# Optimization experiments

Measured on AMD Instinct MI355X. Metric: run time of the kernel, lower is better.

Reference implementation:

```python
import jax, jax.numpy as jnp
import numpy as np

N_FILTERS = 1024
KH, KW = 5, 5
LOC = 3                      # locality (pad + maxpool kernel/stride)
B, H, W = 1024, 64, 64
WIN = KH + 2 * LOC           # 11: sliced window side after padding


def setup_inputs() -> dict:
    key = jax.random.key(0)
    k1, k2, k3, k4 = jax.random.split(key, 4)
    X = jax.random.normal(k1, (B, 1, H, W), dtype=jnp.float32)
    weight = jax.random.normal(k2, (N_FILTERS, 1, KH, KW), dtype=jnp.float32)
    bias = jax.random.normal(k3, (N_FILTERS,), dtype=jnp.float32)
    # top-left corner (i, j) of each filter's window in the padded image;
    # must satisfy i + KH + 2*LOC <= H + 2*LOC  =>  i in [0, H-KH]
    positions = jax.random.randint(k4, (N_FILTERS, 2), 0, H - KH + 1, dtype=jnp.int32)
    return {"X": X, "weight": weight, "bias": bias, "positions": positions}


def reference(X, weight, bias, positions):
    # ZeroPad2d(locality)
    Xp = jnp.pad(X, ((0, 0), (0, 0), (LOC, LOC), (LOC, LOC)))

    def slice_one(pos):
        return jax.lax.dynamic_slice(Xp, (0, 0, pos[0], pos[1]), (B, 1, WIN, WIN))

    windows = jax.vmap(slice_one)(positions)
    lhs = jnp.transpose(windows[:, :, 0], (1, 0, 2, 3))

    # All n_filters tiny single-channel convs as ONE grouped conv.
    conv = jax.lax.conv_general_dilated(
        lhs, weight, window_strides=(1, 1), padding='VALID',
        dimension_numbers=('NCHW', 'OIHW', 'NCHW'),
        feature_group_count=N_FILTERS)                # [B,F,2L+1,2L+1] = [B,F,7,7]
    conv = conv + bias[None, :, None, None]

    # MaxPool2d((LOC,LOC)) with default stride=LOC, floor mode -> 2x2.
    pooled = jax.lax.reduce_window(
        conv, -jnp.inf, jax.lax.max,
        window_dimensions=(1, 1, LOC, LOC),
        window_strides=(1, 1, LOC, LOC),
        padding='VALID')                              # [B,F,2,2]

    # torch.cat(dim=1) over per-filter [B,1,2,2] tensors + reshape(B,-1)
    return pooled.reshape(B, -1)                      # [B, F*4]
```

## Files before the change

### kernel.cpp

```cpp
#include <hip/hip_runtime.h>

#define N_FILTERS 1024
#define B_TOTAL   1024
#define IMG       64
#define PAD_DIM   70

__global__ void zero_border_kernel(_Float16* __restrict__ Xt) {
    int bid = blockIdx.x;
    int r, c;
    if (bid < 420) {
        int r6 = bid / 70;
        c = bid - r6 * 70;
        r = (r6 < 3) ? r6 : r6 + 64;
    } else {
        int t = bid - 420;
        r = 3 + t / 6;
        int k = t - (t / 6) * 6;
        c = (k < 3) ? k : k + 64;
    }
    const size_t pp = (size_t)r * PAD_DIM + c;
    const int bg = threadIdx.x >> 5, l = threadIdx.x & 31;
    unsigned long long* q = (unsigned long long*)Xt
        + (size_t)bg * (4900ull * 32) + pp * 32 + l;
    *q = 0ull;
}

__global__ __launch_bounds__(256) void transpose_kernel(
    const float* __restrict__ X, _Float16* __restrict__ Xt)
{
    __shared__ float T[64 * 65];
    const int pt = blockIdx.x & 63;
    const int bt = blockIdx.x >> 6;
    const int tx = threadIdx.x & 63, ty = threadIdx.x >> 6;

    #pragma unroll
    for (int pass = 0; pass < 16; ++pass) {
        int bl = pass * 4 + ty;
        T[bl * 65 + tx] = X[(size_t)(bt * 64 + bl) * 4096 + pt * 64 + tx];
    }
    __syncthreads();
    #pragma unroll
    for (int pass = 0; pass < 16; ++pass) {
        int pl = pass * 4 + ty;
        int p  = pt * 64 + pl;
        int r  = p >> 6, c = p & 63;
        Xt[((size_t)(bt >> 1) * 4900 + (size_t)(r + 3) * PAD_DIM + (c + 3)) * 128
           + (bt & 1) * 64 + tx] = (_Float16)T[tx * 65 + pl];
    }
}


#define LOAD_ROW(buf, WR) do {                                                  \
    const _Float16* rp_ = Xg + (size_t)((si + (WR)) * PAD_DIM + sj) * 128;      \
    _Pragma("unroll")                                                           \
    for (int wc = 0; wc < 10; ++wc) buf[wc] = rp_[wc * 128];                    \
} while (0)

#define COMPUTE_ROW(buf, WR) do {                                               \
    float in_[10];                                                              \
    _Pragma("unroll")                                                           \
    for (int wc = 0; wc < 10; ++wc) in_[wc] = (float)buf[wc];                   \
    _Pragma("unroll")                                                           \
    for (int y = 0; y < 6; ++y) {                                               \
        if (y >= (((WR) > 4) ? ((WR) - 4) : 0) && y <= (((WR) < 5) ? (WR) : 5)) { \
            const int rr = (WR) - y;                                            \
            _Pragma("unroll")                                                   \
            for (int x = 0; x < 6; ++x) {                                       \
                float s_ = acc[y * 6 + x];                                      \
                _Pragma("unroll")                                               \
                for (int c = 0; c < 5; ++c)                                     \
                    s_ = fmaf(wk[rr * 5 + c], in_[x + c], s_);                  \
                acc[y * 6 + x] = s_;                                            \
            }                                                                   \
        }                                                                       \
    }                                                                           \
    if ((WR) >= 4) {                                                            \
        const int fy = (WR) - 4;                                                \
        _Pragma("unroll")                                                       \
        for (int px = 0; px < 2; ++px) {                                        \
            float m_ = fmaxf(fmaxf(acc[fy * 6 + 3 * px],                        \
                                   acc[fy * 6 + 3 * px + 1]),                   \
                             acc[fy * 6 + 3 * px + 2]);                         \
            const int pi = ((fy >= 3) ? 2 : 0) + px;                            \
            pmax[pi] = fmaxf(pmax[pi], m_);                                     \
        }                                                                       \
    }                                                                           \
} while (0)

__global__ __launch_bounds__(256) void filters_main(
    const _Float16* __restrict__ Xt,
    const float*    __restrict__ W,
    const float*    __restrict__ bias,
    const int*      __restrict__ pos,
    float4*         __restrict__ out4)
{
    const int t    = threadIdx.x;
    const int lane = t & 63;
    const int w    = t >> 6;
    const int bid  = blockIdx.x;
    const int xcd  = bid & 7;
    const int m    = bid >> 3;
    const int bgr  = xcd * 2 + (m & 1);
    const int fg   = m >> 1;

    const int f  = fg * 4 + w;
    const int sf = __builtin_amdgcn_readfirstlane(f);
    const int si = __builtin_amdgcn_readfirstlane(pos[2 * sf]);
    const int sj = __builtin_amdgcn_readfirstlane(pos[2 * sf + 1]);

    float wk[25];
    const float* wp = W + sf * 25;
    #pragma unroll
    for (int k = 0; k < 25; ++k) wk[k] = wp[k];

    const _Float16* Xg = Xt + (size_t)xcd * (4900ull * 128) + (bgr & 1) * 64 + lane;

    float acc[36];
    #pragma unroll
    for (int k = 0; k < 36; ++k) acc[k] = 0.0f;
    float pmax[4];
    #pragma unroll
    for (int k = 0; k < 4; ++k) pmax[k] = -__builtin_inff();

    _Float16 bufA[10], bufB[10];
    LOAD_ROW(bufA, 0);
    LOAD_ROW(bufB, 1);  COMPUTE_ROW(bufA, 0);
    LOAD_ROW(bufA, 2);  COMPUTE_ROW(bufB, 1);
    LOAD_ROW(bufB, 3);  COMPUTE_ROW(bufA, 2);
    LOAD_ROW(bufA, 4);  COMPUTE_ROW(bufB, 3);
    LOAD_ROW(bufB, 5);  COMPUTE_ROW(bufA, 4);
    LOAD_ROW(bufA, 6);  COMPUTE_ROW(bufB, 5);
    LOAD_ROW(bufB, 7);  COMPUTE_ROW(bufA, 6);
    LOAD_ROW(bufA, 8);  COMPUTE_ROW(bufB, 7);
    LOAD_ROW(bufB, 9);  COMPUTE_ROW(bufA, 8);
                        COMPUTE_ROW(bufB, 9);

    const float bv = bias[sf];
    __shared__ float S[4][64][5];
    #pragma unroll
    for (int k = 0; k < 4; ++k) S[w][lane][k] = pmax[k] + bv;
    __syncthreads();

    const int r = t >> 2, q = t & 3;
    float4 val;
    val.x = S[q][r][0];
    val.y = S[q][r][1];
    val.z = S[q][r][2];
    val.w = S[q][r][3];
    out4[(size_t)(bgr * 64 + r) * 1024 + (fg * 4 + q)] = val;
}

extern "C" void kernel_launch(void* const* d_in, const int* in_sizes, int n_in,
                              void* d_out, int out_size, void* d_ws, size_t ws_size,
                              hipStream_t stream) {
    const float* X    = (const float*)d_in[0];
    const float* W    = (const float*)d_in[1];
    const float* bias = (const float*)d_in[2];
    const int*   pos  = (const int*)d_in[3];
    float4* out4 = (float4*)d_out;
    _Float16* Xt = (_Float16*)d_ws;

    zero_border_kernel<<<804, 256, 0, stream>>>(Xt);
    transpose_kernel<<<1024, 256, 0, stream>>>(X, Xt);
    filters_main<<<4096, 256, 0, stream>>>(Xt, W, bias, pos, out4);
}
```

Measured before the change: 110.0 us.

## Process two images per lane with packed float2 math and merge prep kernels

Each lane now loads half2 pairs and computes two batch images together using float2 vector FMAs (packed FMA on CDNA), halving the filters_main grid. The border-zeroing and transpose kernels are fused into one launch, and accumulator/pool initialisation is replaced by first-write assignment. This cuts launch overhead and instruction count per output, at the cost of more registers per thread (72 accumulator floats), which may lower occupancy.

Measured after the change: 97.55 us. 11.3% less time.

```diff
diff --git a/kernel.cpp b/kernel.cpp
--- a/kernel.cpp
+++ b/kernel.cpp
@@ -5,32 +5,37 @@
 #define IMG       64
 #define PAD_DIM   70
 
-__global__ void zero_border_kernel(_Float16* __restrict__ Xt) {
-    int bid = blockIdx.x;
-    int r, c;
-    if (bid < 420) {
-        int r6 = bid / 70;
-        c = bid - r6 * 70;
-        r = (r6 < 3) ? r6 : r6 + 64;
-    } else {
-        int t = bid - 420;
-        r = 3 + t / 6;
-        int k = t - (t / 6) * 6;
-        c = (k < 3) ? k : k + 64;
-    }
-    const size_t pp = (size_t)r * PAD_DIM + c;
-    const int bg = threadIdx.x >> 5, l = threadIdx.x & 31;
-    unsigned long long* q = (unsigned long long*)Xt
-        + (size_t)bg * (4900ull * 32) + pp * 32 + l;
-    *q = 0ull;
-}
+typedef _Float16 half2_t __attribute__((ext_vector_type(2)));
+typedef float    fvec2  __attribute__((ext_vector_type(2)));
 
-__global__ __launch_bounds__(256) void transpose_kernel(
+__global__ __launch_bounds__(256) void prep_kernel(
     const float* __restrict__ X, _Float16* __restrict__ Xt)
 {
+    const int bid = blockIdx.x;
+    if (bid >= 1024) {
+        int pb = bid - 1024;
+        int r, c;
+        if (pb < 420) {
+            int r6 = pb / 70;
+            c = pb - r6 * 70;
+            r = (r6 < 3) ? r6 : r6 + 64;
+        } else {
+            int q = pb - 420;
+            r = 3 + q / 6;
+            int k = q - (q / 6) * 6;
+            c = (k < 3) ? k : k + 64;
+        }
+        const size_t pp = (size_t)r * PAD_DIM + c;
+        const int bg = threadIdx.x >> 5, l = threadIdx.x & 31;
+        unsigned long long* qp = (unsigned long long*)Xt
+            + (size_t)bg * (4900ull * 32) + pp * 32 + l;
+        *qp = 0ull;
+        return;
+    }
+
     __shared__ float T[64 * 65];
-    const int pt = blockIdx.x & 63;
-    const int bt = blockIdx.x >> 6;
+    const int pt = bid & 63;
+    const int bt = bid >> 6;
     const int tx = threadIdx.x & 63, ty = threadIdx.x >> 6;
 
     #pragma unroll
@@ -39,69 +44,91 @@
         T[bl * 65 + tx] = X[(size_t)(bt * 64 + bl) * 4096 + pt * 64 + tx];
     }
     __syncthreads();
+
+    const int h = threadIdx.x & 31;
+    const int v = threadIdx.x >> 5;
+    half2_t* Xt2 = (half2_t*)Xt;
     #pragma unroll
-    for (int pass = 0; pass < 16; ++pass) {
-        int pl = pass * 4 + ty;
+    for (int pass = 0; pass < 8; ++pass) {
+        int pl = pass * 8 + v;
         int p  = pt * 64 + pl;
         int r  = p >> 6, c = p & 63;
-        Xt[((size_t)(bt >> 1) * 4900 + (size_t)(r + 3) * PAD_DIM + (c + 3)) * 128
-           + (bt & 1) * 64 + tx] = (_Float16)T[tx * 65 + pl];
+        half2_t val;
+        val.x = (_Float16)T[(2 * h) * 65 + pl];
+        val.y = (_Float16)T[(2 * h + 1) * 65 + pl];
+        Xt2[((size_t)(bt >> 1) * 4900 + (size_t)(r + 3) * PAD_DIM + (c + 3)) * 64
+            + (bt & 1) * 32 + h] = val;
     }
 }
 
 
 #define LOAD_ROW(buf, WR) do {                                                  \
-    const _Float16* rp_ = Xg + (size_t)((si + (WR)) * PAD_DIM + sj) * 128;      \
+    const half2_t* rp_ = Xg + (size_t)((si + (WR)) * PAD_DIM + sj) * 64;        \
     _Pragma("unroll")                                                           \
-    for (int wc = 0; wc < 10; ++wc) buf[wc] = rp_[wc * 128];                    \
+    for (int wc = 0; wc < 10; ++wc) buf[wc] = rp_[wc * 64];                     \
 } while (0)
 
 #define COMPUTE_ROW(buf, WR) do {                                               \
-    float in_[10];                                                              \
+    fvec2 in_[10];                                                              \
     _Pragma("unroll")                                                           \
-    for (int wc = 0; wc < 10; ++wc) in_[wc] = (float)buf[wc];                   \
+    for (int wc = 0; wc < 10; ++wc) {                                           \
+        in_[wc].x = (float)buf[wc].x;                                           \
+        in_[wc].y = (float)buf[wc].y;                                           \
+    }                                                                           \
     _Pragma("unroll")                                                           \
     for (int y = 0; y < 6; ++y) {                                               \
-        if (y >= (((WR) > 4) ? ((WR) - 4) : 0) && y <= (((WR) < 5) ? (WR) : 5)) { \
-            const int rr = (WR) - y;                                            \
+        if (y >= (((WR) > 4) ? ((WR) - 4) : 0) && y <= (WR)) {                  \
             _Pragma("unroll")                                                   \
             for (int x = 0; x < 6; ++x) {                                       \
-                float s_ = acc[y * 6 + x];                                      \
-                _Pragma("unroll")                                               \
-                for (int c = 0; c < 5; ++c)                                     \
-                    s_ = fmaf(wk[rr * 5 + c], in_[x + c], s_);                  \
-                acc[y * 6 + x] = s_;                                            \
+                if (y == (WR)) {                 \
+                    fvec2 s_ = wk[0] * in_[x];                                  \
+                    _Pragma("unroll")                                           \
+                    for (int c = 1; c < 5; ++c) s_ = wk[c] * in_[x + c] + s_;   \
+                    acc[y * 6 + x] = s_;                                        \
+                } else {                                                        \
+                    const int rr = (WR) - y;                                    \
+                    fvec2 s_ = acc[y * 6 + x];                                  \
+                    _Pragma("unroll")                                           \
+                    for (int c = 0; c < 5; ++c)                                 \
+                        s_ = wk[rr * 5 + c] * in_[x + c] + s_;                  \
+                    acc[y * 6 + x] = s_;                                        \
+                }                                                               \
             }                                                                   \
         }                                                                       \
     }                                                                           \
-    if ((WR) >= 4) {                                                            \
+    if ((WR) >= 4) {                         \
         const int fy = (WR) - 4;                                                \
         _Pragma("unroll")                                                       \
         for (int px = 0; px < 2; ++px) {                                        \
-            float m_ = fmaxf(fmaxf(acc[fy * 6 + 3 * px],                        \
-                                   acc[fy * 6 + 3 * px + 1]),                   \
-                             acc[fy * 6 + 3 * px + 2]);                         \
+            fvec2 a0 = acc[fy * 6 + 3 * px];                                    \
+            fvec2 a1 = acc[fy * 6 + 3 * px + 1];                                \
+            fvec2 a2 = acc[fy * 6 + 3 * px + 2];                                \
+            fvec2 m_;                                                           \
+            m_.x = fmaxf(fmaxf(a0.x, a1.x), a2.x);                              \
+            m_.y = fmaxf(fmaxf(a0.y, a1.y), a2.y);                              \
             const int pi = ((fy >= 3) ? 2 : 0) + px;                            \
-            pmax[pi] = fmaxf(pmax[pi], m_);                                     \
+            if (fy == 0 || fy == 3) {             \
+                pmax[pi] = m_;                                                  \
+            } else {                                                            \
+                pmax[pi].x = fmaxf(pmax[pi].x, m_.x);                           \
+                pmax[pi].y = fmaxf(pmax[pi].y, m_.y);                           \
+            }                                                                   \
         }                                                                       \
     }                                                                           \
 } while (0)
 
 __global__ __launch_bounds__(256) void filters_main(
-    const _Float16* __restrict__ Xt,
-    const float*    __restrict__ W,
-    const float*    __restrict__ bias,
-    const int*      __restrict__ pos,
-    float4*         __restrict__ out4)
+    const half2_t* __restrict__ Xt2,
+    const float*   __restrict__ W,
+    const float*   __restrict__ bias,
+    const int*     __restrict__ pos,
+    float4*        __restrict__ out4)
 {
     const int t    = threadIdx.x;
     const int lane = t & 63;
     const int w    = t >> 6;
-    const int bid  = blockIdx.x;
-    const int xcd  = bid & 7;
-    const int m    = bid >> 3;
-    const int bgr  = xcd * 2 + (m & 1);
-    const int fg   = m >> 1;
+    const int bg   = blockIdx.x & 7;
+    const int fg   = blockIdx.x >> 3;
 
     const int f  = fg * 4 + w;
     const int sf = __builtin_amdgcn_readfirstlane(f);
@@ -113,16 +140,12 @@
     #pragma unroll
     for (int k = 0; k < 25; ++k) wk[k] = wp[k];
 
-    const _Float16* Xg = Xt + (size_t)xcd * (4900ull * 128) + (bgr & 1) * 64 + lane;
+    const half2_t* Xg = Xt2 + (size_t)bg * (4900ull * 64) + lane;
 
-    float acc[36];
-    #pragma unroll
-    for (int k = 0; k < 36; ++k) acc[k] = 0.0f;
-    float pmax[4];
-    #pragma unroll
-    for (int k = 0; k < 4; ++k) pmax[k] = -__builtin_inff();
+    fvec2 acc[36];
+    fvec2 pmax[4];
 
-    _Float16 bufA[10], bufB[10];
+    half2_t bufA[10], bufB[10];
     LOAD_ROW(bufA, 0);
     LOAD_ROW(bufB, 1);  COMPUTE_ROW(bufA, 0);
     LOAD_ROW(bufA, 2);  COMPUTE_ROW(bufB, 1);
@@ -136,18 +159,25 @@
                         COMPUTE_ROW(bufB, 9);
 
     const float bv = bias[sf];
-    __shared__ float S[4][64][5];
+    __shared__ float S[4][128][5];
     #pragma unroll
-    for (int k = 0; k < 4; ++k) S[w][lane][k] = pmax[k] + bv;
+    for (int k = 0; k < 4; ++k) {
+        S[w][2 * lane][k]     = pmax[k].x + bv;
+        S[w][2 * lane + 1][k] = pmax[k].y + bv;
+    }
     __syncthreads();
 
-    const int r = t >> 2, q = t & 3;
-    float4 val;
-    val.x = S[q][r][0];
-    val.y = S[q][r][1];
-    val.z = S[q][r][2];
-    val.w = S[q][r][3];
-    out4[(size_t)(bgr * 64 + r) * 1024 + (fg * 4 + q)] = val;
+    const int q = t & 3, r0 = t >> 2;
+    #pragma unroll
+    for (int half = 0; half < 2; ++half) {
+        const int b = r0 + half * 64;
+        float4 val;
+        val.x = S[q][b][0];
+        val.y = S[q][b][1];
+        val.z = S[q][b][2];
+        val.w = S[q][b][3];
+        out4[(size_t)(bg * 128 + b) * 1024 + fg * 4 + q] = val;
+    }
 }
 
 extern "C" void kernel_launch(void* const* d_in, const int* in_sizes, int n_in,
@@ -160,7 +190,6 @@
     float4* out4 = (float4*)d_out;
     _Float16* Xt = (_Float16*)d_ws;
 
-    zero_border_kernel<<<804, 256, 0, stream>>>(Xt);
-    transpose_kernel<<<1024, 256, 0, stream>>>(X, Xt);
-    filters_main<<<4096, 256, 0, stream>>>(Xt, W, bias, pos, out4);
+    prep_kernel<<<1024 + 804, 256, 0, stream>>>(X, Xt);
+    filters_main<<<2048, 256, 0, stream>>>((const half2_t*)Xt, W, bias, pos, out4);
 }
```
